# Performance work log

Measured on AMD Instinct MI355X. Metric: run time of the kernel, lower is better.

Reference implementation:

```python
import jax, jax.numpy as jnp
import numpy as np

E = 65536      # num edges
T = 262144     # num triplets
H = 128        # hidden_channels
D = 64         # int_emb_size
C = 8          # basis_emb_size
NR = 6         # num_radial
NS = 7         # num_spherical
NB = 6         # len(bt_list) = num_BT + 1
BT_LIST = (-1, 0, 1, 2, 3, 4)
NBS = 1        # num_before_skip (also used for after-skip list in original code)


def setup_inputs() -> dict:
    key = jax.random.key(0)
    ks = iter(jax.random.split(key, 40))
    s = 0.05
    p = lambda shape: jax.random.normal(next(ks), shape, dtype=jnp.float32) * s
    inp = dict(
        x=jax.random.normal(next(ks), (E, H), dtype=jnp.float32),
        rbf=jax.random.normal(next(ks), (E, NR), dtype=jnp.float32),
        sbf=jax.random.normal(next(ks), (T, NS * NR), dtype=jnp.float32),
        idx_kj=jax.random.randint(next(ks), (T,), 0, E),
        idx_ji=jax.random.randint(next(ks), (T,), 0, E),
        bt=jax.random.randint(next(ks), (E,), 0, 5),
        lambda_d=1,
        alpha=jnp.float32(0.7),
        # per-branch stacked weights (6 branches)
        W_kj=p((NB, H, H)), b_kj=jnp.zeros((NB, H), jnp.float32),
        W_rbf1=p((NB, NR, C)), W_rbf2=p((NB, C, H)),
        W_sbf1=p((NB, NS * NR, C)), W_sbf2=p((NB, C, D)),
        W_down=p((NB, H, D)),
        W_ji=p((H, H)), b_ji=jnp.zeros((H,), jnp.float32),
        W_up=p((D, H)),
        rb1_w=p((NBS, H, H)), rb1_b=jnp.zeros((NBS, H), jnp.float32),
        rb2_w=p((NBS, H, H)), rb2_b=jnp.zeros((NBS, H), jnp.float32),
        W_lin=p((H, H)), b_lin=jnp.zeros((H,), jnp.float32),
        ra1_w=p((NBS, H, H)), ra1_b=jnp.zeros((NBS, H), jnp.float32),
        ra2_w=p((NBS, H, H)), ra2_b=jnp.zeros((NBS, H), jnp.float32),
    )
    return inp


def reference(x, rbf, sbf, idx_kj, idx_ji, bt, lambda_d, alpha,
              W_kj, b_kj, W_rbf1, W_rbf2, W_sbf1, W_sbf2, W_down,
              W_ji, b_ji, W_up, rb1_w, rb1_b, rb2_w, rb2_b,
              W_lin, b_lin, ra1_w, ra1_b, ra2_w, ra2_b):
    act = jax.nn.silu

    x_ji = act(x @ W_ji + b_ji)                                  # [E,H]

    # per-branch edge transforms, vectorized over the 6 branches (axis b)
    tmp = act(jnp.einsum('eh,bhg->beg', x, W_kj) + b_kj[:, None, :])   # [B,E,H]
    rbf_p = jnp.einsum('er,brc->bec', rbf, W_rbf1)                     # [B,E,C]
    rbf_p = jnp.einsum('bec,bcg->beg', rbf_p, W_rbf2)                  # [B,E,H]
    tmp = tmp * rbf_p
    down = act(jnp.einsum('beh,bhd->bed', tmp, W_down))                # [B,E,D]

    sbf_p = jnp.einsum('ts,bsc->btc', sbf, W_sbf1)                     # [B,T,C]
    sbf_p = jnp.einsum('btc,bcd->btd', sbf_p, W_sbf2)                  # [B,T,D]

    spe = down[:, idx_kj, :] * sbf_p                                   # [B,T,D]

    # last branch scattered with weight alpha
    x_kj_tot = alpha * jax.ops.segment_sum(spe[-1], idx_ji, num_segments=E)

    # per band-type masked scatter with weight (1 - alpha)
    bt_trip = bt[idx_kj]                                               # [T]
    for b, btv in enumerate(BT_LIST):
        m = (bt_trip == btv).astype(x.dtype)[:, None]
        x_kj_tot = x_kj_tot + (1.0 - alpha) * jax.ops.segment_sum(
            spe[b] * m, idx_ji, num_segments=E)

    x_kj = act(x_kj_tot @ W_up)                                        # [E,H]
    h = x_ji + x_kj
    for i in range(rb1_w.shape[0]):
        h = h + act(act(h @ rb1_w[i] + rb1_b[i]) @ rb2_w[i] + rb2_b[i])
    h = act(h @ W_lin + b_lin) + x
    for i in range(ra1_w.shape[0]):
        h = h + act(act(h @ ra1_w[i] + ra1_b[i]) @ ra2_w[i] + ra2_b[i])
    return h
```

## Files before the change

### kernel.cpp

```cpp
#include <hip/hip_runtime.h>
#include <hip/hip_bf16.h>
#include <stdint.h>

typedef __bf16 bf16_t;
typedef bf16_t bf16x8 __attribute__((ext_vector_type(8)));
typedef bf16_t bf16x2 __attribute__((ext_vector_type(2)));
typedef float f32x4 __attribute__((ext_vector_type(4)));

#define E_N 65536
#define T_N 262144
#define CAP 16
#define OVF_MAX T_N

__device__ __forceinline__ float silu_f(float v) {
  return v / (1.0f + __expf(-v));
}

__device__ __forceinline__ int permrow(int n) {
  return (n & ~31) | ((n & 1) << 4) | ((n & 30) >> 1);
}

__device__ __forceinline__ uint32_t pack_bf16(float a, float b) {
  union { bf16x2 h; uint32_t u; } u;
  u.h[0] = (bf16_t)a; u.h[1] = (bf16_t)b;
  return u.u;
}

template<int KI, int NTJ>
__device__ __forceinline__ void gemm_tile(const bf16_t* A, const bf16_t* B,
                                          int mb, int nb, int l16, int q,
                                          f32x4 (&acc)[2][NTJ]) {
#pragma unroll
  for (int kt = 0; kt < KI; ++kt) {
    const int sw = ((kt * 4 + q) ^ l16) << 3;
    bf16x8 a0 = *(const bf16x8*)(A + ((mb + l16) << 7) + sw);
    bf16x8 a1 = *(const bf16x8*)(A + ((mb + 16 + l16) << 7) + sw);
#pragma unroll
    for (int tj = 0; tj < NTJ; ++tj) {
      bf16x8 b = *(const bf16x8*)(B + ((nb + tj * 16 + l16) << 7) + sw);
      acc[0][tj] = __builtin_amdgcn_mfma_f32_16x16x32_bf16(a0, b, acc[0][tj], 0, 0, 0);
      acc[1][tj] = __builtin_amdgcn_mfma_f32_16x16x32_bf16(a1, b, acc[1][tj], 0, 0, 0);
    }
  }
}

template<int ROWS, int K8>
__device__ __forceinline__ void load_wT(bf16_t* dst, const bf16_t* src, int tid) {
  const uint4* s = (const uint4*)src;
#pragma unroll
  for (int i = tid; i < ROWS * K8; i += 256) {
    const int n = i / K8, k8 = i % K8;
    const int row = permrow(n);
    *(uint4*)(dst + (row << 7) + ((k8 ^ (row & 15)) << 3)) = s[i];
  }
}

template<int C4>
__device__ __forceinline__ void stage_x(bf16_t* dst, const float* src, int tid) {
  const float4* g = (const float4*)src;
#pragma unroll
  for (int i = tid; i < 64 * C4; i += 256) {
    const int row = i / C4, c4 = i % C4;
    float4 v = g[i];
    bf16_t t[4] = {(bf16_t)v.x, (bf16_t)v.y, (bf16_t)v.z, (bf16_t)v.w};
    *(uint2*)(dst + (row << 7) + ((((c4 >> 1) ^ (row & 15)) << 3) | ((c4 & 1) << 2))) =
        *(const uint2*)t;
  }
}

__global__ void prep_kernel(
    const float* __restrict__ W_ji, const float* __restrict__ W_kj,
    const float* __restrict__ W_down, const float* __restrict__ W_up,
    const float* __restrict__ rb1, const float* __restrict__ rb2,
    const float* __restrict__ W_lin, const float* __restrict__ ra1,
    const float* __restrict__ ra2, const float* __restrict__ W_rbf1,
    const float* __restrict__ W_rbf2,
    bf16_t* __restrict__ wjiT, bf16_t* __restrict__ wkjT,
    bf16_t* __restrict__ wdownT, bf16_t* __restrict__ wupT,
    bf16_t* __restrict__ rb1T, bf16_t* __restrict__ rb2T,
    bf16_t* __restrict__ linT, bf16_t* __restrict__ ra1T,
    bf16_t* __restrict__ ra2T, bf16_t* __restrict__ wcb)
{
  const int tid = threadIdx.x;
  if (blockIdx.x >= 112) {
    const int o = (blockIdx.x - 112) * 256 + tid;
    if (o < 640) {
      const int b = o >> 7, n = o & 127;
      bf16_t t[8];
#pragma unroll
      for (int r = 0; r < 6; ++r) {
        const float* w1 = W_rbf1 + (b + 1) * 48 + r * 8;
        const float* w2 = W_rbf2 + (b + 1) * 1024 + n;
        float s = 0.f;
#pragma unroll
        for (int c = 0; c < 8; ++c) s += w1[c] * w2[c * 128];
        t[r] = (bf16_t)s;
      }
      t[6] = (bf16_t)0.f; t[7] = (bf16_t)0.f;
      *(uint4*)(wcb + (b * 128 + n) * 8) = *(const uint4*)t;
    }
    return;
  }
  const int c = blockIdx.x * 256 + tid;
  const float* src; bf16_t* dst; int n, k8, N, K;
  if (c < 22528) {
    const int m = c >> 11, w = c & 2047;
    n = w >> 4; k8 = w & 15; N = 128; K = 128;
    if (m == 0)      { src = W_ji;  dst = wjiT; }
    else if (m <= 5) { src = W_kj + m * 16384; dst = wkjT + (m - 1) * 16384; }
    else if (m == 6) { src = rb1;   dst = rb1T; }
    else if (m == 7) { src = rb2;   dst = rb2T; }
    else if (m == 8) { src = W_lin; dst = linT; }
    else if (m == 9) { src = ra1;   dst = ra1T; }
    else             { src = ra2;   dst = ra2T; }
  } else if (c < 27648) {
    const int m = (c - 22528) >> 10, w = (c - 22528) & 1023;
    n = w >> 4; k8 = w & 15; N = 64; K = 128;
    src = W_down + (m + 1) * 8192; dst = wdownT + m * 8192;
  } else {
    const int w = c - 27648;
    n = w >> 3; k8 = w & 7; N = 128; K = 64;
    src = W_up; dst = wupT;
  }
  bf16_t t[8];
#pragma unroll
  for (int j = 0; j < 8; ++j) t[j] = (bf16_t)src[(k8 * 8 + j) * N + n];
  *(uint4*)(dst + n * K + k8 * 8) = *(const uint4*)t;
}

__global__ __launch_bounds__(256, 2)
void edge_kernel(const float* __restrict__ x, const float* __restrict__ rbf,
                 const float* __restrict__ b_kj, const float* __restrict__ b_ji,
                 const bf16_t* __restrict__ wjiT, const bf16_t* __restrict__ wkjT,
                 const bf16_t* __restrict__ wdownT, const bf16_t* __restrict__ wcb,
                 bf16_t* __restrict__ x_ji_out, bf16_t* __restrict__ down)
{
  __shared__ bf16_t xA[64 * 128];
  __shared__ bf16_t Wb[128 * 128];
  __shared__ bf16_t tmpA[64 * 128];
  __shared__ float biasS[128];
  bf16_t* const rbfA = tmpA;
  bf16_t* const WcB  = tmpA + 64 * 40;

  const int tid = threadIdx.x;
  const int lane = tid & 63, wv = tid >> 6;
  const int q = lane >> 4, l16 = lane & 15;
  const int mb = (wv >> 1) * 32, nb = (wv & 1) * 64;
  const int R = blockIdx.x * 64;
  const int br = blockIdx.y;

  stage_x<32>(xA, x + (size_t)R * 128, tid);
  if (br == 0) {
    load_wT<128, 16>(Wb, wjiT, tid);
    if (tid < 128) biasS[tid] = b_ji[tid];
  } else {
    load_wT<128, 16>(Wb, wkjT + (br - 1) * 16384, tid);
    if (tid < 128) biasS[tid] = b_kj[br * 128 + tid];
    const uint4 z = {0, 0, 0, 0};
    if (tid < 64) {
      const float* rg = rbf + (size_t)(R + tid) * 6;
      bf16_t t[8] = {(bf16_t)rg[0], (bf16_t)rg[1], (bf16_t)rg[2],
                     (bf16_t)rg[3], (bf16_t)rg[4], (bf16_t)rg[5],
                     (bf16_t)0.f, (bf16_t)0.f};
      *(uint4*)(rbfA + tid * 40)      = *(const uint4*)t;
      *(uint4*)(rbfA + tid * 40 + 8)  = z;
      *(uint4*)(rbfA + tid * 40 + 16) = z;
      *(uint4*)(rbfA + tid * 40 + 24) = z;
    } else if (tid >= 128) {
      const int n = tid - 128;
      const int row = permrow(n);
      uint4 w = ((const uint4*)(wcb + (size_t)(br - 1) * 1024))[n];
      *(uint4*)(WcB + row * 40)      = w;
      *(uint4*)(WcB + row * 40 + 8)  = z;
      *(uint4*)(WcB + row * 40 + 16) = z;
      *(uint4*)(WcB + row * 40 + 24) = z;
    }
  }
  __syncthreads();

  f32x4 acc[2][4] = {};
  gemm_tile<4, 4>(xA, Wb, mb, nb, l16, q, acc);

  if (br == 0) {
#pragma unroll
    for (int ti = 0; ti < 2; ++ti)
#pragma unroll
      for (int r = 0; r < 4; ++r) {
        const int row = mb + ti * 16 + q * 4 + r;
#pragma unroll
        for (int gl = 0; gl < 2; ++gl) {
          const int col0 = nb + gl * 32 + 2 * l16;
          const float2 b2 = *(const float2*)&biasS[col0];
          *(uint32_t*)&x_ji_out[(size_t)(R + row) * 128 + col0] =
              pack_bf16(silu_f(acc[ti][2 * gl][r] + b2.x),
                        silu_f(acc[ti][2 * gl + 1][r] + b2.y));
        }
      }
    return;
  }

  f32x4 accr[2][4] = {};
  {
    bf16x8 a0 = *(const bf16x8*)(rbfA + (mb + l16) * 40 + q * 8);
    bf16x8 a1 = *(const bf16x8*)(rbfA + (mb + 16 + l16) * 40 + q * 8);
#pragma unroll
    for (int tj = 0; tj < 4; ++tj) {
      bf16x8 b = *(const bf16x8*)(WcB + (nb + tj * 16 + l16) * 40 + q * 8);
      accr[0][tj] = __builtin_amdgcn_mfma_f32_16x16x32_bf16(a0, b, accr[0][tj], 0, 0, 0);
      accr[1][tj] = __builtin_amdgcn_mfma_f32_16x16x32_bf16(a1, b, accr[1][tj], 0, 0, 0);
    }
  }
  __syncthreads();

#pragma unroll
  for (int ti = 0; ti < 2; ++ti)
#pragma unroll
    for (int r = 0; r < 4; ++r) {
      const int row = mb + ti * 16 + q * 4 + r;
#pragma unroll
      for (int gl = 0; gl < 2; ++gl) {
        const int col0 = nb + gl * 32 + 2 * l16;
        const float2 b2 = *(const float2*)&biasS[col0];
        const float v0 = silu_f(acc[ti][2 * gl][r] + b2.x) * accr[ti][2 * gl][r];
        const float v1 = silu_f(acc[ti][2 * gl + 1][r] + b2.y) * accr[ti][2 * gl + 1][r];
        *(uint32_t*)&tmpA[(row << 7) + ((((col0 >> 3) ^ (row & 15)) << 3) | (col0 & 7))] =
            pack_bf16(v0, v1);
      }
    }
  __syncthreads();
  load_wT<64, 16>(xA, wdownT + (br - 1) * 8192, tid);
  __syncthreads();

  const int nb2 = (wv & 1) * 32;
  f32x4 acc2[2][2] = {};
  gemm_tile<4, 2>(tmpA, xA, mb, nb2, l16, q, acc2);
#pragma unroll
  for (int ti = 0; ti < 2; ++ti)
#pragma unroll
    for (int r = 0; r < 4; ++r) {
      const int row = mb + ti * 16 + q * 4 + r;
      const int col0 = nb2 + 2 * l16;
      *(uint32_t*)&down[((size_t)(br - 1) * E_N + R + row) * 64 + col0] =
          pack_bf16(silu_f(acc2[ti][0][r]), silu_f(acc2[ti][1][r]));
    }
}

__global__ __launch_bounds__(256, 4)
void c8_kernel(const float* __restrict__ sbf, const int* __restrict__ idx_kj,
               const int* __restrict__ idx_ji, const int* __restrict__ bt,
               const float* __restrict__ Wsbf1,
               float* __restrict__ c8g, uint32_t* __restrict__ meta,
               int* __restrict__ cnt, int* __restrict__ list,
               int* __restrict__ ovf)
{
  __shared__ float s_sbf[64 * 44];
  __shared__ float s_W1[2016];
  __shared__ float s_c8[64 * 16];
  __shared__ int s_bs[64];

  const int tid = threadIdx.x;
  const int base = blockIdx.x * 64;

  for (int i = tid; i < 2016; i += 256) s_W1[i] = Wsbf1[i];
  if (tid < 64) {
    const int t = base + tid;
    const int kj = idx_kj[t];
    const int ji = idx_ji[t];
    const int bs = bt[kj] + 1;
    s_bs[tid] = bs;
    meta[t] = (uint32_t)kj | ((uint32_t)bs << 16);
    const int pos = atomicAdd(&cnt[ji], 1);
    if (pos < CAP) {
      list[ji * CAP + pos] = t;
    } else {
      const int o = atomicAdd(&ovf[0], 1);
      if (o < OVF_MAX) { ovf[2 + 2 * o] = t; ovf[2 + 2 * o + 1] = ji; }
    }
  }
  {
    const float2* sg = (const float2*)(sbf + (size_t)base * 42);
    for (int i = tid; i < 64 * 21; i += 256) {
      const int r = i / 21, c2 = i - r * 21;
      const float2 v = sg[i];
      s_sbf[r * 44 + c2 * 2] = v.x;
      s_sbf[r * 44 + c2 * 2 + 1] = v.y;
    }
  }
  __syncthreads();

  {
    const int i = tid >> 2;
    const int brr = (tid >> 1) & 1;
    const int cg = tid & 1;
    const int b = brr ? s_bs[i] : 5;
    const float* w = &s_W1[b * 336 + cg * 4];
    const float* sb = &s_sbf[i * 44];
    float a0 = 0.f, a1 = 0.f, a2 = 0.f, a3 = 0.f;
#pragma unroll
    for (int s = 0; s < 42; ++s) {
      const float sv = sb[s];
      const float* ws = w + s * 8;
      a0 += sv * ws[0]; a1 += sv * ws[1]; a2 += sv * ws[2]; a3 += sv * ws[3];
    }
    float* dc = &s_c8[i * 16 + brr * 8 + cg * 4];
    dc[0] = a0; dc[1] = a1; dc[2] = a2; dc[3] = a3;
  }
  __syncthreads();

  {
    const float4* s4 = (const float4*)s_c8;
    float4* g4 = (float4*)(c8g + (size_t)base * 16);
    g4[tid] = s4[tid];
  }
}

__global__ __launch_bounds__(256, 8)
void gather_kernel(const int* __restrict__ cnt, const int* __restrict__ list,
                   const uint32_t* __restrict__ meta, const float* __restrict__ c8g,
                   const float* __restrict__ Wsbf2, const bf16_t* __restrict__ down,
                   const float* __restrict__ alpha_p, const int* __restrict__ ovf,
                   float* __restrict__ xkj)
{
  __shared__ float sW2[3072];
  for (int i = threadIdx.x; i < 3072; i += 256) sW2[i] = Wsbf2[i];
  __syncthreads();

  const int e = blockIdx.x * 4 + (threadIdx.x >> 6);
  const int j = threadIdx.x & 63;
  const float alpha = alpha_p[0], oma = 1.f - alpha;
  const float* w5 = &sW2[5 * 512 + j];

  float acc = 0.f;
  int n = cnt[e];
  if (n > CAP) n = CAP;
#pragma unroll 2
  for (int k = 0; k < n; ++k) {
    const int t = __builtin_amdgcn_readfirstlane(list[e * CAP + k]);
    const uint32_t m = __builtin_amdgcn_readfirstlane(meta[t]);
    const int kj = m & 0xffff;
    const int b  = m >> 16;
    const float g5 = (float)down[((size_t)4 * E_N + kj) * 64 + j];
    const float gb = (float)down[((size_t)(b - 1) * E_N + kj) * 64 + j];
    const float* cp = c8g + (size_t)t * 16;
    float d5 = 0.f, db = 0.f;
#pragma unroll
    for (int c = 0; c < 8; ++c) {
      d5 += cp[c]     * w5[c * 64];
      db += cp[8 + c] * sW2[b * 512 + c * 64 + j];
    }
    acc += alpha * g5 * d5 + oma * gb * db;
  }

  const int oc = ovf[0];
  for (int k = 0; k < oc; ++k) {
    const int ji = ovf[2 + 2 * k + 1];
    if (ji != e) continue;
    const int t = ovf[2 + 2 * k];
    const uint32_t m = meta[t];
    const int kj = m & 0xffff;
    const int b  = m >> 16;
    const float g5 = (float)down[((size_t)4 * E_N + kj) * 64 + j];
    const float gb = (float)down[((size_t)(b - 1) * E_N + kj) * 64 + j];
    const float* cp = c8g + (size_t)t * 16;
    float d5 = 0.f, db = 0.f;
#pragma unroll
    for (int c = 0; c < 8; ++c) {
      d5 += cp[c]     * w5[c * 64];
      db += cp[8 + c] * sW2[b * 512 + c * 64 + j];
    }
    acc += alpha * g5 * d5 + oma * gb * db;
  }

  xkj[(size_t)e * 64 + j] = acc;
}

__global__ __launch_bounds__(256, 2)
void epi_kernel(const float* __restrict__ x, const bf16_t* __restrict__ x_ji,
                const float* __restrict__ xkj,
                const bf16_t* __restrict__ wupT,
                const bf16_t* __restrict__ rb1T, const float* __restrict__ rb1_b,
                const bf16_t* __restrict__ rb2T, const float* __restrict__ rb2_b,
                const bf16_t* __restrict__ linT, const float* __restrict__ lin_b,
                const bf16_t* __restrict__ ra1T, const float* __restrict__ ra1_b,
                const bf16_t* __restrict__ ra2T, const float* __restrict__ ra2_b,
                float* __restrict__ out)
{
  __shared__ bf16_t bufA[64 * 128];
  __shared__ bf16_t bufB[64 * 128];
  __shared__ bf16_t Wb[128 * 128];
  __shared__ float biasS[128];

  const int tid = threadIdx.x;
  const int lane = tid & 63, wv = tid >> 6;
  const int q = lane >> 4, l16 = lane & 15;
  const int mb = (wv >> 1) * 32, nb = (wv & 1) * 64;
  const int R = blockIdx.x * 64;

  stage_x<16>(bufA, xkj + (size_t)R * 64, tid);
  load_wT<128, 8>(Wb, wupT, tid);
  __syncthreads();

  f32x4 hreg[2][4];
  {
    f32x4 acc[2][4] = {};
    gemm_tile<2, 4>(bufA, Wb, mb, nb, l16, q, acc);
#pragma unroll
    for (int ti = 0; ti < 2; ++ti)
#pragma unroll
      for (int r = 0; r < 4; ++r) {
        const int row = mb + ti * 16 + q * 4 + r;
#pragma unroll
        for (int gl = 0; gl < 2; ++gl) {
          const int col0 = nb + gl * 32 + 2 * l16;
          union { uint32_t u; bf16x2 h; } xj;
          xj.u = *(const uint32_t*)&x_ji[(size_t)(R + row) * 128 + col0];
          const float h0 = (float)xj.h[0] + silu_f(acc[ti][2 * gl][r]);
          const float h1 = (float)xj.h[1] + silu_f(acc[ti][2 * gl + 1][r]);
          hreg[ti][2 * gl][r] = h0;
          hreg[ti][2 * gl + 1][r] = h1;
          *(uint32_t*)&bufB[(row << 7) + ((((col0 >> 3) ^ (row & 15)) << 3) | (col0 & 7))] =
              pack_bf16(h0, h1);
        }
      }
  }

#define EPI_STAGE(ASRC, WSRC, BIAS, BODY)                                        \
  __syncthreads();                                                               \
  load_wT<128, 16>(Wb, WSRC, tid);                                               \
  if (tid < 128) biasS[tid] = BIAS[tid];                                         \
  __syncthreads();                                                               \
  {                                                                              \
    f32x4 acc[2][4] = {};                                                        \
    gemm_tile<4, 4>(ASRC, Wb, mb, nb, l16, q, acc);                              \
    _Pragma("unroll")                                                            \
    for (int ti = 0; ti < 2; ++ti)                                               \
      _Pragma("unroll")                                                          \
      for (int r = 0; r < 4; ++r) {                                              \
        const int row = mb + ti * 16 + q * 4 + r;                                \
        _Pragma("unroll")                                                        \
        for (int gl = 0; gl < 2; ++gl) {                                         \
          const int col0 = nb + gl * 32 + 2 * l16;                               \
          const float2 b2 = *(const float2*)&biasS[col0];                        \
          const float g0 = acc[ti][2 * gl][r] + b2.x;                            \
          const float g1 = acc[ti][2 * gl + 1][r] + b2.y;                        \
          BODY                                                                   \
        }                                                                        \
      }                                                                          \
  }

  EPI_STAGE(bufB, rb1T, rb1_b, {
    *(uint32_t*)&bufA[(row << 7) + ((((col0 >> 3) ^ (row & 15)) << 3) | (col0 & 7))] =
        pack_bf16(silu_f(g0), silu_f(g1));
  })

  EPI_STAGE(bufA, rb2T, rb2_b, {
    const float h0 = hreg[ti][2 * gl][r] + silu_f(g0);
    const float h1 = hreg[ti][2 * gl + 1][r] + silu_f(g1);
    hreg[ti][2 * gl][r] = h0; hreg[ti][2 * gl + 1][r] = h1;
    *(uint32_t*)&bufB[(row << 7) + ((((col0 >> 3) ^ (row & 15)) << 3) | (col0 & 7))] =
        pack_bf16(h0, h1);
  })

  EPI_STAGE(bufB, linT, lin_b, {
    const float2 xv = *(const float2*)&x[(size_t)(R + row) * 128 + col0];
    const float h0 = silu_f(g0) + xv.x;
    const float h1 = silu_f(g1) + xv.y;
    hreg[ti][2 * gl][r] = h0; hreg[ti][2 * gl + 1][r] = h1;
    *(uint32_t*)&bufA[(row << 7) + ((((col0 >> 3) ^ (row & 15)) << 3) | (col0 & 7))] =
        pack_bf16(h0, h1);
  })

  EPI_STAGE(bufA, ra1T, ra1_b, {
    *(uint32_t*)&bufB[(row << 7) + ((((col0 >> 3) ^ (row & 15)) << 3) | (col0 & 7))] =
        pack_bf16(silu_f(g0), silu_f(g1));
  })

  EPI_STAGE(bufB, ra2T, ra2_b, {
    float2 o;
    o.x = hreg[ti][2 * gl][r] + silu_f(g0);
    o.y = hreg[ti][2 * gl + 1][r] + silu_f(g1);
    *(float2*)&out[(size_t)(R + row) * 128 + col0] = o;
  })
#undef EPI_STAGE
}

extern "C" void kernel_launch(void* const* d_in, const int* in_sizes, int n_in,
                              void* d_out, int out_size, void* d_ws, size_t ws_size,
                              hipStream_t stream)
{
  (void)in_sizes; (void)n_in; (void)out_size; (void)ws_size;
  const float* x      = (const float*)d_in[0];
  const float* rbf    = (const float*)d_in[1];
  const float* sbf    = (const float*)d_in[2];
  const int*   idx_kj = (const int*)d_in[3];
  const int*   idx_ji = (const int*)d_in[4];
  const int*   bt     = (const int*)d_in[5];
  const float* alpha  = (const float*)d_in[7];
  const float* W_kj   = (const float*)d_in[8];
  const float* b_kj   = (const float*)d_in[9];
  const float* W_rbf1 = (const float*)d_in[10];
  const float* W_rbf2 = (const float*)d_in[11];
  const float* W_sbf1 = (const float*)d_in[12];
  const float* W_sbf2 = (const float*)d_in[13];
  const float* W_down = (const float*)d_in[14];
  const float* W_ji   = (const float*)d_in[15];
  const float* b_ji   = (const float*)d_in[16];
  const float* W_up   = (const float*)d_in[17];
  const float* rb1_w  = (const float*)d_in[18];
  const float* rb1_b  = (const float*)d_in[19];
  const float* rb2_w  = (const float*)d_in[20];
  const float* rb2_b  = (const float*)d_in[21];
  const float* W_lin  = (const float*)d_in[22];
  const float* b_lin  = (const float*)d_in[23];
  const float* ra1_w  = (const float*)d_in[24];
  const float* ra1_b  = (const float*)d_in[25];
  const float* ra2_w  = (const float*)d_in[26];
  const float* ra2_b  = (const float*)d_in[27];

  char* ws = (char*)d_ws;
  bf16_t* down   = (bf16_t*)(ws);
  bf16_t* x_ji   = (bf16_t*)(ws + 41943040);
  float*  xkj    = (float*) (ws + 58720256);
  char* wbase    = ws + 75497472;
  bf16_t* wjiT   = (bf16_t*)(wbase + 0);
  bf16_t* wkjT   = (bf16_t*)(wbase + 32768);
  bf16_t* wdownT = (bf16_t*)(wbase + 196608);
  bf16_t* wupT   = (bf16_t*)(wbase + 278528);
  bf16_t* rb1T   = (bf16_t*)(wbase + 294912);
  bf16_t* rb2T   = (bf16_t*)(wbase + 327680);
  bf16_t* linT   = (bf16_t*)(wbase + 360448);
  bf16_t* ra1T   = (bf16_t*)(wbase + 393216);
  bf16_t* ra2T   = (bf16_t*)(wbase + 425984);
  bf16_t* wcb    = (bf16_t*)(wbase + 458752);
  float*    c8g  = (float*)   (ws + 75966464);
  uint32_t* meta = (uint32_t*)(ws + 92743680);
  int*      list = (int*)     (ws + 93792256);
  int*      cnt  = (int*)     (ws + 97986560);
  int*      ovf  = (int*)     (ws + 98248704);

  hipMemsetAsync(cnt, 0, 262144 + 8, stream);
  prep_kernel<<<115, 256, 0, stream>>>(W_ji, W_kj, W_down, W_up, rb1_w, rb2_w,
                                       W_lin, ra1_w, ra2_w, W_rbf1, W_rbf2,
                                       wjiT, wkjT, wdownT, wupT, rb1T, rb2T,
                                       linT, ra1T, ra2T, wcb);
  edge_kernel<<<dim3(E_N / 64, 6), 256, 0, stream>>>(x, rbf, b_kj, b_ji, wjiT,
                                                     wkjT, wdownT, wcb, x_ji, down);
  c8_kernel<<<T_N / 64, 256, 0, stream>>>(sbf, idx_kj, idx_ji, bt, W_sbf1,
                                          c8g, meta, cnt, list, ovf);
  gather_kernel<<<E_N / 4 / 64, 256, 0, stream>>>(cnt, list, meta, c8g, W_sbf2,
                                                  down, alpha, ovf, xkj);
  epi_kernel<<<E_N / 64, 256, 0, stream>>>(x, x_ji, xkj, wupT, rb1T, rb1_b,
                                           rb2T, rb2_b, linT, b_lin,
                                           ra1T, ra1_b, ra2T, ra2_b,
                                           (float*)d_out);
}
```

Before: 340.9 us.

## Merge edge and c8 kernels into one launch with interleaved block roles

Combines the edge GEMM kernel and the sbf/c8 triplet kernel into a single launch of 10240 blocks. Out of every five blocks, three do edge work and two do c8 work, and the two roles share shared memory through a union. The goal is to run the compute-heavy MFMA edge work alongside the memory- and atomic-heavy triplet work, and to remove one launch boundary. In exchange, the c8 blocks now run with the edge kernel's launch bounds and shared-memory footprint, which may lower their occupancy.

```diff
diff --git a/kernel.cpp b/kernel.cpp
--- a/kernel.cpp
+++ b/kernel.cpp
@@ -129,59 +129,112 @@
 }
 
 __global__ __launch_bounds__(256, 2)
-void edge_kernel(const float* __restrict__ x, const float* __restrict__ rbf,
-                 const float* __restrict__ b_kj, const float* __restrict__ b_ji,
-                 const bf16_t* __restrict__ wjiT, const bf16_t* __restrict__ wkjT,
-                 const bf16_t* __restrict__ wdownT, const bf16_t* __restrict__ wcb,
-                 bf16_t* __restrict__ x_ji_out, bf16_t* __restrict__ down)
+void edge_c8_kernel(const float* __restrict__ x, const float* __restrict__ rbf,
+                    const float* __restrict__ b_kj, const float* __restrict__ b_ji,
+                    const bf16_t* __restrict__ wjiT, const bf16_t* __restrict__ wkjT,
+                    const bf16_t* __restrict__ wdownT, const bf16_t* __restrict__ wcb,
+                    bf16_t* __restrict__ x_ji_out, bf16_t* __restrict__ down,
+                    const float* __restrict__ sbf, const int* __restrict__ idx_kj,
+                    const int* __restrict__ idx_ji, const int* __restrict__ bt,
+                    const float* __restrict__ Wsbf1,
+                    float* __restrict__ c8g, uint32_t* __restrict__ meta,
+                    int* __restrict__ cnt, int* __restrict__ list,
+                    int* __restrict__ ovf)
 {
-  __shared__ bf16_t xA[64 * 128];
-  __shared__ bf16_t Wb[128 * 128];
-  __shared__ bf16_t tmpA[64 * 128];
-  __shared__ float biasS[128];
-  bf16_t* const rbfA = tmpA;
-  bf16_t* const WcB  = tmpA + 64 * 40;
+  __shared__ union {
+    struct {
+      bf16_t xA[64 * 128];
+      bf16_t Wb[128 * 128];
+      bf16_t tmpA[64 * 128];
+      float biasS[128];
+    } e;
+    struct {
+      float s_sbf[64 * 44];
+      float s_W1[2016];
+      float s_c8[64 * 16];
+      int s_bs[64];
+    } c;
+  } S;
 
   const int tid = threadIdx.x;
-  const int lane = tid & 63, wv = tid >> 6;
-  const int q = lane >> 4, l16 = lane & 15;
-  const int mb = (wv >> 1) * 32, nb = (wv & 1) * 64;
-  const int R = blockIdx.x * 64;
-  const int br = blockIdx.y;
-
-  stage_x<32>(xA, x + (size_t)R * 128, tid);
-  if (br == 0) {
-    load_wT<128, 16>(Wb, wjiT, tid);
-    if (tid < 128) biasS[tid] = b_ji[tid];
-  } else {
-    load_wT<128, 16>(Wb, wkjT + (br - 1) * 16384, tid);
-    if (tid < 128) biasS[tid] = b_kj[br * 128 + tid];
-    const uint4 z = {0, 0, 0, 0};
-    if (tid < 64) {
-      const float* rg = rbf + (size_t)(R + tid) * 6;
-      bf16_t t[8] = {(bf16_t)rg[0], (bf16_t)rg[1], (bf16_t)rg[2],
-                     (bf16_t)rg[3], (bf16_t)rg[4], (bf16_t)rg[5],
-                     (bf16_t)0.f, (bf16_t)0.f};
-      *(uint4*)(rbfA + tid * 40)      = *(const uint4*)t;
-      *(uint4*)(rbfA + tid * 40 + 8)  = z;
-      *(uint4*)(rbfA + tid * 40 + 16) = z;
-      *(uint4*)(rbfA + tid * 40 + 24) = z;
-    } else if (tid >= 128) {
-      const int n = tid - 128;
-      const int row = permrow(n);
-      uint4 w = ((const uint4*)(wcb + (size_t)(br - 1) * 1024))[n];
-      *(uint4*)(WcB + row * 40)      = w;
-      *(uint4*)(WcB + row * 40 + 8)  = z;
-      *(uint4*)(WcB + row * 40 + 16) = z;
-      *(uint4*)(WcB + row * 40 + 24) = z;
-    }
-  }
-  __syncthreads();
-
-  f32x4 acc[2][4] = {};
-  gemm_tile<4, 4>(xA, Wb, mb, nb, l16, q, acc);
-
-  if (br == 0) {
+  const int bid = blockIdx.x;
+  const int g = bid / 5, m5 = bid % 5;
+
+  if (m5 < 3) {
+    const int eb = g * 3 + m5;
+    const int br = eb % 6;
+    const int R = (eb / 6) * 64;
+
+    bf16_t* const rbfA = S.e.tmpA;
+    bf16_t* const WcB  = S.e.tmpA + 64 * 40;
+
+    const int lane = tid & 63, wv = tid >> 6;
+    const int q = lane >> 4, l16 = lane & 15;
+    const int mb = (wv >> 1) * 32, nb = (wv & 1) * 64;
+
+    stage_x<32>(S.e.xA, x + (size_t)R * 128, tid);
+    if (br == 0) {
+      load_wT<128, 16>(S.e.Wb, wjiT, tid);
+      if (tid < 128) S.e.biasS[tid] = b_ji[tid];
+    } else {
+      load_wT<128, 16>(S.e.Wb, wkjT + (br - 1) * 16384, tid);
+      if (tid < 128) S.e.biasS[tid] = b_kj[br * 128 + tid];
+      const uint4 z = {0, 0, 0, 0};
+      if (tid < 64) {
+        const float* rg = rbf + (size_t)(R + tid) * 6;
+        bf16_t t[8] = {(bf16_t)rg[0], (bf16_t)rg[1], (bf16_t)rg[2],
+                       (bf16_t)rg[3], (bf16_t)rg[4], (bf16_t)rg[5],
+                       (bf16_t)0.f, (bf16_t)0.f};
+        *(uint4*)(rbfA + tid * 40)      = *(const uint4*)t;
+        *(uint4*)(rbfA + tid * 40 + 8)  = z;
+        *(uint4*)(rbfA + tid * 40 + 16) = z;
+        *(uint4*)(rbfA + tid * 40 + 24) = z;
+      } else if (tid >= 128) {
+        const int n = tid - 128;
+        const int row = permrow(n);
+        uint4 w = ((const uint4*)(wcb + (size_t)(br - 1) * 1024))[n];
+        *(uint4*)(WcB + row * 40)      = w;
+        *(uint4*)(WcB + row * 40 + 8)  = z;
+        *(uint4*)(WcB + row * 40 + 16) = z;
+        *(uint4*)(WcB + row * 40 + 24) = z;
+      }
+    }
+    __syncthreads();
+
+    f32x4 acc[2][4] = {};
+    gemm_tile<4, 4>(S.e.xA, S.e.Wb, mb, nb, l16, q, acc);
+
+    if (br == 0) {
+#pragma unroll
+      for (int ti = 0; ti < 2; ++ti)
+#pragma unroll
+        for (int r = 0; r < 4; ++r) {
+          const int row = mb + ti * 16 + q * 4 + r;
+#pragma unroll
+          for (int gl = 0; gl < 2; ++gl) {
+            const int col0 = nb + gl * 32 + 2 * l16;
+            const float2 b2 = *(const float2*)&S.e.biasS[col0];
+            *(uint32_t*)&x_ji_out[(size_t)(R + row) * 128 + col0] =
+                pack_bf16(silu_f(acc[ti][2 * gl][r] + b2.x),
+                          silu_f(acc[ti][2 * gl + 1][r] + b2.y));
+          }
+        }
+      return;
+    }
+
+    f32x4 accr[2][4] = {};
+    {
+      bf16x8 a0 = *(const bf16x8*)(rbfA + (mb + l16) * 40 + q * 8);
+      bf16x8 a1 = *(const bf16x8*)(rbfA + (mb + 16 + l16) * 40 + q * 8);
+#pragma unroll
+      for (int tj = 0; tj < 4; ++tj) {
+        bf16x8 b = *(const bf16x8*)(WcB + (nb + tj * 16 + l16) * 40 + q * 8);
+        accr[0][tj] = __builtin_amdgcn_mfma_f32_16x16x32_bf16(a0, b, accr[0][tj], 0, 0, 0);
+        accr[1][tj] = __builtin_amdgcn_mfma_f32_16x16x32_bf16(a1, b, accr[1][tj], 0, 0, 0);
+      }
+    }
+    __syncthreads();
+
 #pragma unroll
     for (int ti = 0; ti < 2; ++ti)
 #pragma unroll
@@ -190,127 +243,87 @@
 #pragma unroll
         for (int gl = 0; gl < 2; ++gl) {
           const int col0 = nb + gl * 32 + 2 * l16;
-          const float2 b2 = *(const float2*)&biasS[col0];
-          *(uint32_t*)&x_ji_out[(size_t)(R + row) * 128 + col0] =
-              pack_bf16(silu_f(acc[ti][2 * gl][r] + b2.x),
-                        silu_f(acc[ti][2 * gl + 1][r] + b2.y));
+          const float2 b2 = *(const float2*)&S.e.biasS[col0];
+          const float v0 = silu_f(acc[ti][2 * gl][r] + b2.x) * accr[ti][2 * gl][r];
+          const float v1 = silu_f(acc[ti][2 * gl + 1][r] + b2.y) * accr[ti][2 * gl + 1][r];
+          *(uint32_t*)&S.e.tmpA[(row << 7) + ((((col0 >> 3) ^ (row & 15)) << 3) | (col0 & 7))] =
+              pack_bf16(v0, v1);
         }
       }
+    __syncthreads();
+    load_wT<64, 16>(S.e.xA, wdownT + (br - 1) * 8192, tid);
+    __syncthreads();
+
+    const int nb2 = (wv & 1) * 32;
+    f32x4 acc2[2][2] = {};
+    gemm_tile<4, 2>(S.e.tmpA, S.e.xA, mb, nb2, l16, q, acc2);
+#pragma unroll
+    for (int ti = 0; ti < 2; ++ti)
+#pragma unroll
+      for (int r = 0; r < 4; ++r) {
+        const int row = mb + ti * 16 + q * 4 + r;
+        const int col0 = nb2 + 2 * l16;
+        *(uint32_t*)&down[((size_t)(br - 1) * E_N + R + row) * 64 + col0] =
+            pack_bf16(silu_f(acc2[ti][0][r]), silu_f(acc2[ti][1][r]));
+      }
     return;
   }
 
-  f32x4 accr[2][4] = {};
   {
-    bf16x8 a0 = *(const bf16x8*)(rbfA + (mb + l16) * 40 + q * 8);
-    bf16x8 a1 = *(const bf16x8*)(rbfA + (mb + 16 + l16) * 40 + q * 8);
-#pragma unroll
-    for (int tj = 0; tj < 4; ++tj) {
-      bf16x8 b = *(const bf16x8*)(WcB + (nb + tj * 16 + l16) * 40 + q * 8);
-      accr[0][tj] = __builtin_amdgcn_mfma_f32_16x16x32_bf16(a0, b, accr[0][tj], 0, 0, 0);
-      accr[1][tj] = __builtin_amdgcn_mfma_f32_16x16x32_bf16(a1, b, accr[1][tj], 0, 0, 0);
-    }
-  }
-  __syncthreads();
-
-#pragma unroll
-  for (int ti = 0; ti < 2; ++ti)
-#pragma unroll
-    for (int r = 0; r < 4; ++r) {
-      const int row = mb + ti * 16 + q * 4 + r;
-#pragma unroll
-      for (int gl = 0; gl < 2; ++gl) {
-        const int col0 = nb + gl * 32 + 2 * l16;
-        const float2 b2 = *(const float2*)&biasS[col0];
-        const float v0 = silu_f(acc[ti][2 * gl][r] + b2.x) * accr[ti][2 * gl][r];
-        const float v1 = silu_f(acc[ti][2 * gl + 1][r] + b2.y) * accr[ti][2 * gl + 1][r];
-        *(uint32_t*)&tmpA[(row << 7) + ((((col0 >> 3) ^ (row & 15)) << 3) | (col0 & 7))] =
-            pack_bf16(v0, v1);
-      }
-    }
-  __syncthreads();
-  load_wT<64, 16>(xA, wdownT + (br - 1) * 8192, tid);
-  __syncthreads();
-
-  const int nb2 = (wv & 1) * 32;
-  f32x4 acc2[2][2] = {};
-  gemm_tile<4, 2>(tmpA, xA, mb, nb2, l16, q, acc2);
-#pragma unroll
-  for (int ti = 0; ti < 2; ++ti)
-#pragma unroll
-    for (int r = 0; r < 4; ++r) {
-      const int row = mb + ti * 16 + q * 4 + r;
-      const int col0 = nb2 + 2 * l16;
-      *(uint32_t*)&down[((size_t)(br - 1) * E_N + R + row) * 64 + col0] =
-          pack_bf16(silu_f(acc2[ti][0][r]), silu_f(acc2[ti][1][r]));
-    }
-}
-
-__global__ __launch_bounds__(256, 4)
-void c8_kernel(const float* __restrict__ sbf, const int* __restrict__ idx_kj,
-               const int* __restrict__ idx_ji, const int* __restrict__ bt,
-               const float* __restrict__ Wsbf1,
-               float* __restrict__ c8g, uint32_t* __restrict__ meta,
-               int* __restrict__ cnt, int* __restrict__ list,
-               int* __restrict__ ovf)
-{
-  __shared__ float s_sbf[64 * 44];
-  __shared__ float s_W1[2016];
-  __shared__ float s_c8[64 * 16];
-  __shared__ int s_bs[64];
-
-  const int tid = threadIdx.x;
-  const int base = blockIdx.x * 64;
-
-  for (int i = tid; i < 2016; i += 256) s_W1[i] = Wsbf1[i];
-  if (tid < 64) {
-    const int t = base + tid;
-    const int kj = idx_kj[t];
-    const int ji = idx_ji[t];
-    const int bs = bt[kj] + 1;
-    s_bs[tid] = bs;
-    meta[t] = (uint32_t)kj | ((uint32_t)bs << 16);
-    const int pos = atomicAdd(&cnt[ji], 1);
-    if (pos < CAP) {
-      list[ji * CAP + pos] = t;
-    } else {
-      const int o = atomicAdd(&ovf[0], 1);
-      if (o < OVF_MAX) { ovf[2 + 2 * o] = t; ovf[2 + 2 * o + 1] = ji; }
-    }
-  }
-  {
-    const float2* sg = (const float2*)(sbf + (size_t)base * 42);
-    for (int i = tid; i < 64 * 21; i += 256) {
-      const int r = i / 21, c2 = i - r * 21;
-      const float2 v = sg[i];
-      s_sbf[r * 44 + c2 * 2] = v.x;
-      s_sbf[r * 44 + c2 * 2 + 1] = v.y;
-    }
-  }
-  __syncthreads();
-
-  {
-    const int i = tid >> 2;
-    const int brr = (tid >> 1) & 1;
-    const int cg = tid & 1;
-    const int b = brr ? s_bs[i] : 5;
-    const float* w = &s_W1[b * 336 + cg * 4];
-    const float* sb = &s_sbf[i * 44];
-    float a0 = 0.f, a1 = 0.f, a2 = 0.f, a3 = 0.f;
-#pragma unroll
-    for (int s = 0; s < 42; ++s) {
-      const float sv = sb[s];
-      const float* ws = w + s * 8;
-      a0 += sv * ws[0]; a1 += sv * ws[1]; a2 += sv * ws[2]; a3 += sv * ws[3];
-    }
-    float* dc = &s_c8[i * 16 + brr * 8 + cg * 4];
-    dc[0] = a0; dc[1] = a1; dc[2] = a2; dc[3] = a3;
-  }
-  __syncthreads();
-
-  {
-    const float4* s4 = (const float4*)s_c8;
-    float4* g4 = (float4*)(c8g + (size_t)base * 16);
-    g4[tid] = s4[tid];
+    const int ct = g * 2 + (m5 - 3);
+    const int base = ct * 64;
+
+    for (int i = tid; i < 2016; i += 256) S.c.s_W1[i] = Wsbf1[i];
+    if (tid < 64) {
+      const int t = base + tid;
+      const int kj = idx_kj[t];
+      const int ji = idx_ji[t];
+      const int bs = bt[kj] + 1;
+      S.c.s_bs[tid] = bs;
+      meta[t] = (uint32_t)kj | ((uint32_t)bs << 16);
+      const int pos = atomicAdd(&cnt[ji], 1);
+      if (pos < CAP) {
+        list[ji * CAP + pos] = t;
+      } else {
+        const int o = atomicAdd(&ovf[0], 1);
+        if (o < OVF_MAX) { ovf[2 + 2 * o] = t; ovf[2 + 2 * o + 1] = ji; }
+      }
+    }
+    {
+      const float2* sg = (const float2*)(sbf + (size_t)base * 42);
+      for (int i = tid; i < 64 * 21; i += 256) {
+        const int r = i / 21, c2 = i - r * 21;
+        const float2 v = sg[i];
+        S.c.s_sbf[r * 44 + c2 * 2] = v.x;
+        S.c.s_sbf[r * 44 + c2 * 2 + 1] = v.y;
+      }
+    }
+    __syncthreads();
+
+    {
+      const int i = tid >> 2;
+      const int brr = (tid >> 1) & 1;
+      const int cg = tid & 1;
+      const int b = brr ? S.c.s_bs[i] : 5;
+      const float* w = &S.c.s_W1[b * 336 + cg * 4];
+      const float* sb = &S.c.s_sbf[i * 44];
+      float a0 = 0.f, a1 = 0.f, a2 = 0.f, a3 = 0.f;
+#pragma unroll
+      for (int s = 0; s < 42; ++s) {
+        const float sv = sb[s];
+        const float* ws = w + s * 8;
+        a0 += sv * ws[0]; a1 += sv * ws[1]; a2 += sv * ws[2]; a3 += sv * ws[3];
+      }
+      float* dc = &S.c.s_c8[i * 16 + brr * 8 + cg * 4];
+      dc[0] = a0; dc[1] = a1; dc[2] = a2; dc[3] = a3;
+    }
+    __syncthreads();
+
+    {
+      const float4* s4 = (const float4*)S.c.s_c8;
+      float4* g4 = (float4*)(c8g + (size_t)base * 16);
+      g4[tid] = s4[tid];
+    }
   }
 }
 
@@ -543,10 +556,10 @@
                                        W_lin, ra1_w, ra2_w, W_rbf1, W_rbf2,
                                        wjiT, wkjT, wdownT, wupT, rb1T, rb2T,
                                        linT, ra1T, ra2T, wcb);
-  edge_kernel<<<dim3(E_N / 64, 6), 256, 0, stream>>>(x, rbf, b_kj, b_ji, wjiT,
-                                                     wkjT, wdownT, wcb, x_ji, down);
-  c8_kernel<<<T_N / 64, 256, 0, stream>>>(sbf, idx_kj, idx_ji, bt, W_sbf1,
-                                          c8g, meta, cnt, list, ovf);
+  edge_c8_kernel<<<10240, 256, 0, stream>>>(x, rbf, b_kj, b_ji, wjiT, wkjT,
+                                            wdownT, wcb, x_ji, down,
+                                            sbf, idx_kj, idx_ji, bt, W_sbf1,
+                                            c8g, meta, cnt, list, ovf);
   gather_kernel<<<E_N / 4 / 64, 256, 0, stream>>>(cnt, list, meta, c8g, W_sbf2,
                                                   down, alpha, ovf, xkj);
   epi_kernel<<<E_N / 64, 256, 0, stream>>>(x, x_ji, xkj, wupT, rb1T, rb1_b,
```

After: 388.6 us. 14.0% more time.

## Pre-convert x to swizzled bf16 once and shrink edge kernel shared memory

Applied to the files above, without the earlier changes.

The prep kernel now converts x once into a pre-swizzled bf16 image, stored in the c8g workspace. The edge kernel then copies that image straight into shared memory instead of having each of the six branch blocks re-read and convert the fp32 x. The rank-6 rbf projection moves from a padded MFMA to scalar FMAs on small shared buffers, so the tmp buffer disappears and W_down reuses Wb. This lowers shared memory enough for three blocks per CU, and the grid is flattened so the six branches of a tile launch next to each other for L2 reuse. The cost is an extra write and read of a bf16 copy of x, plus more scalar ALU work in the epilogue.

```diff
diff --git a/kernel.cpp b/kernel.cpp
--- a/kernel.cpp
+++ b/kernel.cpp
@@ -74,16 +74,30 @@
     const float* __restrict__ rb1, const float* __restrict__ rb2,
     const float* __restrict__ W_lin, const float* __restrict__ ra1,
     const float* __restrict__ ra2, const float* __restrict__ W_rbf1,
-    const float* __restrict__ W_rbf2,
+    const float* __restrict__ W_rbf2, const float* __restrict__ x,
     bf16_t* __restrict__ wjiT, bf16_t* __restrict__ wkjT,
     bf16_t* __restrict__ wdownT, bf16_t* __restrict__ wupT,
     bf16_t* __restrict__ rb1T, bf16_t* __restrict__ rb2T,
     bf16_t* __restrict__ linT, bf16_t* __restrict__ ra1T,
-    bf16_t* __restrict__ ra2T, bf16_t* __restrict__ wcb)
+    bf16_t* __restrict__ ra2T, bf16_t* __restrict__ wcb,
+    bf16_t* __restrict__ ximg)
 {
+  __shared__ __align__(16) bf16_t tile[64 * 128];
   const int tid = threadIdx.x;
-  if (blockIdx.x >= 112) {
-    const int o = (blockIdx.x - 112) * 256 + tid;
+  const int blk = blockIdx.x;
+
+  if (blk >= 115) {
+    const int t = blk - 115;
+    stage_x<32>(tile, x + (size_t)t * 8192, tid);
+    __syncthreads();
+    uint4* dst = (uint4*)(ximg + (size_t)t * 8192);
+    const uint4* s = (const uint4*)tile;
+#pragma unroll
+    for (int i = 0; i < 4; ++i) dst[i * 256 + tid] = s[i * 256 + tid];
+    return;
+  }
+  if (blk >= 112) {
+    const int o = (blk - 112) * 256 + tid;
     if (o < 640) {
       const int b = o >> 7, n = o & 127;
       bf16_t t[8];
@@ -101,7 +115,7 @@
     }
     return;
   }
-  const int c = blockIdx.x * 256 + tid;
+  const int c = blk * 256 + tid;
   const float* src; bf16_t* dst; int n, k8, N, K;
   if (c < 22528) {
     const int m = c >> 11, w = c & 2047;
@@ -128,52 +142,49 @@
   *(uint4*)(dst + n * K + k8 * 8) = *(const uint4*)t;
 }
 
-__global__ __launch_bounds__(256, 2)
-void edge_kernel(const float* __restrict__ x, const float* __restrict__ rbf,
+__global__ __launch_bounds__(256, 3)
+void edge_kernel(const bf16_t* __restrict__ ximg, const float* __restrict__ rbf,
                  const float* __restrict__ b_kj, const float* __restrict__ b_ji,
                  const bf16_t* __restrict__ wjiT, const bf16_t* __restrict__ wkjT,
                  const bf16_t* __restrict__ wdownT, const bf16_t* __restrict__ wcb,
                  bf16_t* __restrict__ x_ji_out, bf16_t* __restrict__ down)
 {
-  __shared__ bf16_t xA[64 * 128];
-  __shared__ bf16_t Wb[128 * 128];
-  __shared__ bf16_t tmpA[64 * 128];
+  __shared__ __align__(16) bf16_t xA[64 * 128];
+  __shared__ __align__(16) bf16_t Wb[128 * 128];
+  __shared__ __align__(16) bf16_t wcbS[128 * 8];
+  __shared__ __align__(16) bf16_t rbfS[64 * 8];
   __shared__ float biasS[128];
-  bf16_t* const rbfA = tmpA;
-  bf16_t* const WcB  = tmpA + 64 * 40;
 
   const int tid = threadIdx.x;
   const int lane = tid & 63, wv = tid >> 6;
   const int q = lane >> 4, l16 = lane & 15;
   const int mb = (wv >> 1) * 32, nb = (wv & 1) * 64;
-  const int R = blockIdx.x * 64;
-  const int br = blockIdx.y;
-
-  stage_x<32>(xA, x + (size_t)R * 128, tid);
+  const int eb = blockIdx.x;
+  const int br = eb % 6;
+  const int tile = eb / 6;
+  const int R = tile * 64;
+
+  {
+    const uint4* s = (const uint4*)(ximg + (size_t)tile * 8192);
+    uint4* d = (uint4*)xA;
+#pragma unroll
+    for (int i = 0; i < 4; ++i) d[i * 256 + tid] = s[i * 256 + tid];
+  }
   if (br == 0) {
     load_wT<128, 16>(Wb, wjiT, tid);
     if (tid < 128) biasS[tid] = b_ji[tid];
   } else {
     load_wT<128, 16>(Wb, wkjT + (br - 1) * 16384, tid);
     if (tid < 128) biasS[tid] = b_kj[br * 128 + tid];
-    const uint4 z = {0, 0, 0, 0};
+    if (tid >= 128)
+      ((uint4*)wcbS)[tid - 128] =
+          ((const uint4*)(wcb + (size_t)(br - 1) * 1024))[tid - 128];
     if (tid < 64) {
       const float* rg = rbf + (size_t)(R + tid) * 6;
       bf16_t t[8] = {(bf16_t)rg[0], (bf16_t)rg[1], (bf16_t)rg[2],
                      (bf16_t)rg[3], (bf16_t)rg[4], (bf16_t)rg[5],
                      (bf16_t)0.f, (bf16_t)0.f};
-      *(uint4*)(rbfA + tid * 40)      = *(const uint4*)t;
-      *(uint4*)(rbfA + tid * 40 + 8)  = z;
-      *(uint4*)(rbfA + tid * 40 + 16) = z;
-      *(uint4*)(rbfA + tid * 40 + 24) = z;
-    } else if (tid >= 128) {
-      const int n = tid - 128;
-      const int row = permrow(n);
-      uint4 w = ((const uint4*)(wcb + (size_t)(br - 1) * 1024))[n];
-      *(uint4*)(WcB + row * 40)      = w;
-      *(uint4*)(WcB + row * 40 + 8)  = z;
-      *(uint4*)(WcB + row * 40 + 16) = z;
-      *(uint4*)(WcB + row * 40 + 24) = z;
+      *(uint4*)(rbfS + tid * 8) = *(const uint4*)t;
     }
   }
   __syncthreads();
@@ -199,41 +210,50 @@
     return;
   }
 
-  f32x4 accr[2][4] = {};
-  {
-    bf16x8 a0 = *(const bf16x8*)(rbfA + (mb + l16) * 40 + q * 8);
-    bf16x8 a1 = *(const bf16x8*)(rbfA + (mb + 16 + l16) * 40 + q * 8);
-#pragma unroll
-    for (int tj = 0; tj < 4; ++tj) {
-      bf16x8 b = *(const bf16x8*)(WcB + (nb + tj * 16 + l16) * 40 + q * 8);
-      accr[0][tj] = __builtin_amdgcn_mfma_f32_16x16x32_bf16(a0, b, accr[0][tj], 0, 0, 0);
-      accr[1][tj] = __builtin_amdgcn_mfma_f32_16x16x32_bf16(a1, b, accr[1][tj], 0, 0, 0);
-    }
-  }
-  __syncthreads();
-
+  __syncthreads();
+
+  load_wT<64, 16>(Wb, wdownT + (br - 1) * 8192, tid);
+
+  float wc[2][2][6];
+#pragma unroll
+  for (int gl = 0; gl < 2; ++gl)
+#pragma unroll
+    for (int j = 0; j < 2; ++j) {
+      const int col = nb + gl * 32 + 2 * l16 + j;
+      bf16x8 w8 = *(const bf16x8*)&wcbS[col * 8];
+#pragma unroll
+      for (int c = 0; c < 6; ++c) wc[gl][j][c] = (float)w8[c];
+    }
 #pragma unroll
   for (int ti = 0; ti < 2; ++ti)
 #pragma unroll
     for (int r = 0; r < 4; ++r) {
       const int row = mb + ti * 16 + q * 4 + r;
+      bf16x8 rv8 = *(const bf16x8*)&rbfS[row * 8];
+      float rv[6];
+#pragma unroll
+      for (int c = 0; c < 6; ++c) rv[c] = (float)rv8[c];
 #pragma unroll
       for (int gl = 0; gl < 2; ++gl) {
         const int col0 = nb + gl * 32 + 2 * l16;
         const float2 b2 = *(const float2*)&biasS[col0];
-        const float v0 = silu_f(acc[ti][2 * gl][r] + b2.x) * accr[ti][2 * gl][r];
-        const float v1 = silu_f(acc[ti][2 * gl + 1][r] + b2.y) * accr[ti][2 * gl + 1][r];
-        *(uint32_t*)&tmpA[(row << 7) + ((((col0 >> 3) ^ (row & 15)) << 3) | (col0 & 7))] =
+        float p0 = 0.f, p1 = 0.f;
+#pragma unroll
+        for (int c = 0; c < 6; ++c) {
+          p0 += rv[c] * wc[gl][0][c];
+          p1 += rv[c] * wc[gl][1][c];
+        }
+        const float v0 = silu_f(acc[ti][2 * gl][r] + b2.x) * p0;
+        const float v1 = silu_f(acc[ti][2 * gl + 1][r] + b2.y) * p1;
+        *(uint32_t*)&xA[(row << 7) + ((((col0 >> 3) ^ (row & 15)) << 3) | (col0 & 7))] =
             pack_bf16(v0, v1);
       }
     }
   __syncthreads();
-  load_wT<64, 16>(xA, wdownT + (br - 1) * 8192, tid);
-  __syncthreads();
 
   const int nb2 = (wv & 1) * 32;
   f32x4 acc2[2][2] = {};
-  gemm_tile<4, 2>(tmpA, xA, mb, nb2, l16, q, acc2);
+  gemm_tile<4, 2>(xA, Wb, mb, nb2, l16, q, acc2);
 #pragma unroll
   for (int ti = 0; ti < 2; ++ti)
 #pragma unroll
@@ -385,9 +405,9 @@
                 const bf16_t* __restrict__ ra2T, const float* __restrict__ ra2_b,
                 float* __restrict__ out)
 {
-  __shared__ bf16_t bufA[64 * 128];
-  __shared__ bf16_t bufB[64 * 128];
-  __shared__ bf16_t Wb[128 * 128];
+  __shared__ __align__(16) bf16_t bufA[64 * 128];
+  __shared__ __align__(16) bf16_t bufB[64 * 128];
+  __shared__ __align__(16) bf16_t Wb[128 * 128];
   __shared__ float biasS[128];
 
   const int tid = threadIdx.x;
@@ -537,14 +557,15 @@
   int*      list = (int*)     (ws + 93792256);
   int*      cnt  = (int*)     (ws + 97986560);
   int*      ovf  = (int*)     (ws + 98248704);
+  bf16_t* ximg   = (bf16_t*)c8g;
 
   hipMemsetAsync(cnt, 0, 262144 + 8, stream);
-  prep_kernel<<<115, 256, 0, stream>>>(W_ji, W_kj, W_down, W_up, rb1_w, rb2_w,
-                                       W_lin, ra1_w, ra2_w, W_rbf1, W_rbf2,
-                                       wjiT, wkjT, wdownT, wupT, rb1T, rb2T,
-                                       linT, ra1T, ra2T, wcb);
-  edge_kernel<<<dim3(E_N / 64, 6), 256, 0, stream>>>(x, rbf, b_kj, b_ji, wjiT,
-                                                     wkjT, wdownT, wcb, x_ji, down);
+  prep_kernel<<<1139, 256, 0, stream>>>(W_ji, W_kj, W_down, W_up, rb1_w, rb2_w,
+                                        W_lin, ra1_w, ra2_w, W_rbf1, W_rbf2, x,
+                                        wjiT, wkjT, wdownT, wupT, rb1T, rb2T,
+                                        linT, ra1T, ra2T, wcb, ximg);
+  edge_kernel<<<E_N / 64 * 6, 256, 0, stream>>>(ximg, rbf, b_kj, b_ji, wjiT,
+                                                wkjT, wdownT, wcb, x_ji, down);
   c8_kernel<<<T_N / 64, 256, 0, stream>>>(sbf, idx_kj, idx_ji, bt, W_sbf1,
                                           c8g, meta, cnt, list, ovf);
   gather_kernel<<<E_N / 4 / 64, 256, 0, stream>>>(cnt, list, meta, c8g, W_sbf2,
```

New measurement: 330.2 us. 1.03x faster.
